# Kernel tuning notes

Hardware: AMD Instinct MI355X
Metric: run time of the kernel (lower is better)

The kernel has to match this reference:

```python
import jax, jax.numpy as jnp
import numpy as np
from jax import lax
from jax.scipy.special import logsumexp

NUM_CLASSES = 170
ALPHA = 0.2
B, T = 16, 8192


def setup_inputs() -> dict:
    key = jax.random.key(0)
    logits = jax.random.normal(key, (B, T, NUM_CLASSES), dtype=jnp.float32)
    # transition matrix: alpha on diagonal, uniform off-diagonal
    off = (1.0 - ALPHA) / (NUM_CLASSES - 1)
    trans = jnp.full((NUM_CLASSES, NUM_CLASSES), off, dtype=jnp.float32)
    trans = trans.at[jnp.arange(NUM_CLASSES), jnp.arange(NUM_CLASSES)].set(ALPHA)
    init = jnp.full((NUM_CLASSES,), 1.0 / NUM_CLASSES, dtype=jnp.float32)
    return {"logits": logits, "transition_matrix": trans, "initial_distribution": init}


def reference(logits, transition_matrix, initial_distribution):
    eps = 1e-12
    log_T = jnp.log(transition_matrix + eps)          # (C, C)
    log_init = jnp.log(initial_distribution + eps)    # (C,)
    log_probs = jax.nn.log_softmax(logits, axis=-1)   # (B, T, C)
    Bn, Tn, C = log_probs.shape
    lp = jnp.moveaxis(log_probs, 1, 0)                # (T, B, C) time-major for scan

    # forward recursion: alpha_t[j] = logsumexp_i(alpha_{t-1}[i] + logT[i,j]) + lp_t[j]
    alpha0 = log_init[None, :] + lp[0]                # (B, C)

    def fwd_step(a_prev, lp_t):
        a = logsumexp(a_prev[:, :, None] + log_T[None, :, :], axis=1) + lp_t
        return a, a

    _, alpha_rest = lax.scan(fwd_step, alpha0, lp[1:])
    alpha = jnp.concatenate([alpha0[None], alpha_rest], axis=0)  # (T, B, C)

    # backward recursion: beta_t[i] = logsumexp_j(logT[i,j] + lp_{t+1}[j] + beta_{t+1}[j])
    betaT = jnp.zeros((Bn, C), dtype=log_probs.dtype)

    def bwd_step(b_next, lp_next):
        b = logsumexp(log_T[None, :, :] + (lp_next + b_next)[:, None, :], axis=2)
        return b, b

    _, beta_rest = lax.scan(bwd_step, betaT, lp[1:], reverse=True)
    beta = jnp.concatenate([beta_rest, betaT[None]], axis=0)     # (T, B, C)

    posterior = jax.nn.softmax(alpha + beta, axis=-1)            # (T, B, C)
    return jnp.moveaxis(posterior, 0, 1)                         # (B, T, C)
```

## Files before the change

kernel.cpp:

```cpp
#include <hip/hip_runtime.h>
#include <hip/hip_fp16.h>


#define NCLS 170
#define BB 16
#define TT 8192
#define LCH 32
#define WARM 16
#define NCHUNK (TT / LCH)

struct Row { float x, y, z; };

__device__ __forceinline__ float wave_sum_b(float x) {
  x += __int_as_float(__builtin_amdgcn_update_dpp(0, __float_as_int(x), 0x111, 0xF, 0xF, true));
  x += __int_as_float(__builtin_amdgcn_update_dpp(0, __float_as_int(x), 0x112, 0xF, 0xF, true));
  x += __int_as_float(__builtin_amdgcn_update_dpp(0, __float_as_int(x), 0x114, 0xF, 0xF, true));
  x += __int_as_float(__builtin_amdgcn_update_dpp(0, __float_as_int(x), 0x118, 0xF, 0xF, true));
  x += __int_as_float(__builtin_amdgcn_update_dpp(0, __float_as_int(x), 0x142, 0xA, 0xF, true));
  x += __int_as_float(__builtin_amdgcn_update_dpp(0, __float_as_int(x), 0x143, 0xC, 0xF, true));
  return __int_as_float(__builtin_amdgcn_readlane(__float_as_int(x), 63));
}

__global__ __launch_bounds__(64, 4) void hmm_fb(const float* __restrict__ logits,
                                                const float* __restrict__ trans,
                                                const float* __restrict__ initd,
                                                float* __restrict__ out) {
  __shared__ __half2 pb01[LCH * 64];
  const int lane = threadIdx.x;

  const int d = blockIdx.x;
  const int o = (d & 7) * (BB * NCHUNK / 8) + (d >> 3);
  const int b = o / NCHUNK;
  const int chunk = o % NCHUNK;
  const int t0 = chunk * LCH;
  const int t1 = t0 + LCH;

  const float off = trans[1] + 1e-12f;
  const float dia = trans[0] + 1e-12f;
  const float dd = dia - off;

  const int c0 = lane, c1 = lane + 64, c2 = lane + 128;
  const bool cok = (c2 < NCLS);
  const float* lg = logits + (size_t)b * TT * NCLS;

  auto ldraw = [&](int t) -> Row {
    const float* r = lg + (size_t)t * NCLS;
    Row w;
    w.x = r[c0];
    w.y = r[c1];
    w.z = cok ? r[c2] : 0.f;
    return w;
  };
  auto eRow = [&](const Row& w) -> Row {
    Row e;
    e.x = __expf(w.x);
    e.y = __expf(w.y);
    e.z = cok ? __expf(w.z) : 0.f;
    return e;
  };

  __half2 ph2[LCH / 2];

  float v0, v1, v2s;
  auto fcore = [&](const Row& e, float& u0, float& u1, float& u2) -> float {
    u0 = v0 * e.x; u1 = v1 * e.y; u2 = v2s * e.z;
    float S = wave_sum_b(u0 + u1 + u2);
    float os = off * S;
    v0 = __fmaf_rn(dd, u0, os);
    v1 = __fmaf_rn(dd, u1, os);
    v2s = __fmaf_rn(dd, u2, os);
    return S;
  };

  Row r0, r1, r2, r3;
  if (t0 == 0) {
    v0 = initd[c0]; v1 = initd[c1]; v2s = cok ? initd[c2] : 0.f;
    r0 = ldraw(0); r1 = ldraw(1); r2 = ldraw(2); r3 = ldraw(3);
  } else {
    v0 = 1.f; v1 = 1.f; v2s = cok ? 1.f : 0.f;
    const int ts = t0 - WARM;
    r0 = ldraw(ts); r1 = ldraw(ts + 1); r2 = ldraw(ts + 2); r3 = ldraw(ts + 3);
#pragma unroll
    for (int g = 0; g < WARM / 4; ++g) {
      const int tn = ts + 4 * g + 4;
      Row n0 = ldraw(tn), n1 = ldraw(tn + 1), n2 = ldraw(tn + 2), n3 = ldraw(tn + 3);
      Row e0 = eRow(r0), e1 = eRow(r1), e2 = eRow(r2), e3 = eRow(r3);
      float u0, u1, u2;
      fcore(e0, u0, u1, u2);
      fcore(e1, u0, u1, u2);
      fcore(e2, u0, u1, u2);
      float S3 = fcore(e3, u0, u1, u2);
      float rs = __builtin_amdgcn_rcpf(S3);
      v0 *= rs; v1 *= rs; v2s *= rs;
      r0 = n0; r1 = n1; r2 = n2; r3 = n3;
    }
  }

#define FGROUP(i)                                                              \
  {                                                                            \
    const int tn = t0 + (i) + 4;                                               \
    Row n0 = ldraw(tn + 0 > TT - 1 ? TT - 1 : tn + 0);                         \
    Row n1 = ldraw(tn + 1 > TT - 1 ? TT - 1 : tn + 1);                         \
    Row n2 = ldraw(tn + 2 > TT - 1 ? TT - 1 : tn + 2);                         \
    Row n3 = ldraw(tn + 3 > TT - 1 ? TT - 1 : tn + 3);                         \
    Row e0 = eRow(r0), e1 = eRow(r1), e2 = eRow(r2), e3 = eRow(r3);            \
    float u0, u1, u2;                                                          \
    float S0 = fcore(e0, u0, u1, u2);                                          \
    float x0 = __builtin_amdgcn_rcpf(S0);                                      \
    pb01[((i) + 0) * 64 + lane] = __floats2half2_rn(u0 * x0, u1 * x0);         \
    __half pa = __float2half(u2 * x0);                                         \
    float S1 = fcore(e1, u0, u1, u2);                                          \
    float x1 = __builtin_amdgcn_rcpf(S1);                                      \
    pb01[((i) + 1) * 64 + lane] = __floats2half2_rn(u0 * x1, u1 * x1);         \
    ph2[(i) / 2] = __halves2half2(pa, __float2half(u2 * x1));                  \
    float S2 = fcore(e2, u0, u1, u2);                                          \
    float x2 = __builtin_amdgcn_rcpf(S2);                                      \
    pb01[((i) + 2) * 64 + lane] = __floats2half2_rn(u0 * x2, u1 * x2);         \
    __half pb = __float2half(u2 * x2);                                         \
    float S3 = fcore(e3, u0, u1, u2);                                          \
    float x3 = __builtin_amdgcn_rcpf(S3);                                      \
    pb01[((i) + 3) * 64 + lane] = __floats2half2_rn(u0 * x3, u1 * x3);         \
    ph2[(i) / 2 + 1] = __halves2half2(pb, __float2half(u2 * x3));              \
    v0 *= x3; v1 *= x3; v2s *= x3;          \
    r0 = n0; r1 = n1; r2 = n2; r3 = n3;                                        \
  }

  FGROUP(0) FGROUP(4) FGROUP(8) FGROUP(12)
  FGROUP(16) FGROUP(20) FGROUP(24) FGROUP(28)
#undef FGROUP

  float q0 = 1.f, q1 = 1.f, q2 = cok ? 1.f : 0.f;
  int te2 = t1 + WARM;
  if (te2 > TT) te2 = TT;

  auto ldB = [&](int tp1) -> Row {
    int rr = tp1 < 0 ? 0 : (tp1 > TT - 1 ? TT - 1 : tp1);
    Row w = ldraw(rr);
    if (tp1 >= TT) { w.x = 0.f; w.y = 0.f; w.z = 0.f; }
    return w;
  };
  auto bcore = [&](const Row& e) -> float {
    float w0 = e.x * q0, w1 = e.y * q1, w2 = e.z * q2;
    float S = wave_sum_b(w0 + w1 + w2);
    float os = off * S;
    q0 = __fmaf_rn(dd, w0, os);
    q1 = __fmaf_rn(dd, w1, os);
    q2 = __fmaf_rn(dd, w2, os);
    return S;
  };

  r0 = ldB(te2); r1 = ldB(te2 - 1); r2 = ldB(te2 - 2); r3 = ldB(te2 - 3);

  for (int t = te2 - 1; t > t1 - 1; t -= 4) {
    Row n0 = ldB(t - 3), n1 = ldB(t - 4), n2 = ldB(t - 5), n3 = ldB(t - 6);
    Row e0 = eRow(r0), e1 = eRow(r1), e2 = eRow(r2), e3 = eRow(r3);
    bcore(e0); bcore(e1); bcore(e2);
    float S3 = bcore(e3);
    float rs = __builtin_amdgcn_rcpf(S3);
    q0 *= rs; q1 *= rs; q2 *= rs;
    r0 = n0; r1 = n1; r2 = n2; r3 = n3;
  }

#define WPOST(tt, ta)                                                          \
  {                                                                            \
    __half2 h01 = pb01[(tt) * 64 + lane];                                      \
    float a0 = __low2float(h01) * q0;                                          \
    float a1 = __high2float(h01) * q1;                                         \
    __half2 h2v = ph2[(tt) >> 1];                                              \
    float p2f = ((tt) & 1) ? __high2float(h2v) : __low2float(h2v);             \
    float a2 = cok ? p2f * q2 : 0.f;                                           \
    float z = wave_sum_b(a0 + a1 + a2);                                        \
    float iz = __builtin_amdgcn_rcpf(z);                                       \
    float* op = out + ((size_t)b * TT + (ta)) * NCLS;                          \
    op[c0] = a0 * iz;                                                          \
    op[c1] = a1 * iz;                                                          \
    if (cok) op[c2] = a2 * iz;                                                 \
  }

#define BGROUP(i)                                                              \
  {                                                                            \
    const int t = t1 - 1 - (i);                                                \
    Row n0 = ldB(t - 3), n1 = ldB(t - 4), n2 = ldB(t - 5), n3 = ldB(t - 6);    \
    Row e0 = eRow(r0), e1 = eRow(r1), e2 = eRow(r2), e3 = eRow(r3);            \
    bcore(e0); WPOST(LCH - 1 - (i), t)                                         \
    bcore(e1); WPOST(LCH - 2 - (i), t - 1)                                     \
    bcore(e2); WPOST(LCH - 3 - (i), t - 2)                                     \
    float S3 = bcore(e3); WPOST(LCH - 4 - (i), t - 3)                          \
    float rs = __builtin_amdgcn_rcpf(S3);                                      \
    q0 *= rs; q1 *= rs; q2 *= rs;                                              \
    r0 = n0; r1 = n1; r2 = n2; r3 = n3;                                        \
  }

  BGROUP(0) BGROUP(4) BGROUP(8) BGROUP(12)
  BGROUP(16) BGROUP(20) BGROUP(24) BGROUP(28)
#undef BGROUP
#undef WPOST
}

extern "C" void kernel_launch(void* const* d_in, const int* in_sizes, int n_in,
                              void* d_out, int out_size, void* d_ws, size_t ws_size,
                              hipStream_t stream) {
  const float* logits = (const float*)d_in[0];
  const float* trans  = (const float*)d_in[1];
  const float* initd  = (const float*)d_in[2];
  float* out = (float*)d_out;
  dim3 grid(BB * NCHUNK);
  dim3 block(64);
  hipLaunchKernelGGL(hmm_fb, grid, block, 0, stream, logits, trans, initd, out);
}
```

Baseline: 59.65 us.

## Vectorize row loads/stores as float2 and deepen prefetch to two groups

Changes the class-to-lane mapping so each lane loads and stores classes 2*lane and 2*lane+1 as a single float2, with a scalar tail for classes 128..169. Also doubles the register prefetch depth from one 4-row group to two (a/b rotation) in both the forward and backward passes. Warm-up loops become runtime-bounded, and the load clamps now stay inside the chunk. The goal is fewer memory instructions and more latency hiding on the serial recurrence, at the cost of more registers under launch_bounds(64,4).

```diff
diff --git a/kernel.cpp b/kernel.cpp
--- a/kernel.cpp
+++ b/kernel.cpp
@@ -39,16 +39,16 @@
   const float dia = trans[0] + 1e-12f;
   const float dd = dia - off;
 
-  const int c0 = lane, c1 = lane + 64, c2 = lane + 128;
-  const bool cok = (c2 < NCLS);
+  const bool cok = (lane < NCLS - 128);
   const float* lg = logits + (size_t)b * TT * NCLS;
 
   auto ldraw = [&](int t) -> Row {
     const float* r = lg + (size_t)t * NCLS;
+    float2 xy = *(const float2*)(r + 2 * lane);
     Row w;
-    w.x = r[c0];
-    w.y = r[c1];
-    w.z = cok ? r[c2] : 0.f;
+    w.x = xy.x;
+    w.y = xy.y;
+    w.z = cok ? r[128 + lane] : 0.f;
     return w;
   };
   auto eRow = [&](const Row& w) -> Row {
@@ -72,38 +72,42 @@
     return S;
   };
 
-  Row r0, r1, r2, r3;
+  Row a0, a1, a2, a3, b0, b1, b2, b3;
+  int ts;
   if (t0 == 0) {
-    v0 = initd[c0]; v1 = initd[c1]; v2s = cok ? initd[c2] : 0.f;
-    r0 = ldraw(0); r1 = ldraw(1); r2 = ldraw(2); r3 = ldraw(3);
+    ts = 0;
+    float2 i01 = *(const float2*)(initd + 2 * lane);
+    v0 = i01.x; v1 = i01.y; v2s = cok ? initd[128 + lane] : 0.f;
   } else {
+    ts = t0 - WARM;
     v0 = 1.f; v1 = 1.f; v2s = cok ? 1.f : 0.f;
-    const int ts = t0 - WARM;
-    r0 = ldraw(ts); r1 = ldraw(ts + 1); r2 = ldraw(ts + 2); r3 = ldraw(ts + 3);
-#pragma unroll
-    for (int g = 0; g < WARM / 4; ++g) {
-      const int tn = ts + 4 * g + 4;
-      Row n0 = ldraw(tn), n1 = ldraw(tn + 1), n2 = ldraw(tn + 2), n3 = ldraw(tn + 3);
-      Row e0 = eRow(r0), e1 = eRow(r1), e2 = eRow(r2), e3 = eRow(r3);
-      float u0, u1, u2;
-      fcore(e0, u0, u1, u2);
-      fcore(e1, u0, u1, u2);
-      fcore(e2, u0, u1, u2);
-      float S3 = fcore(e3, u0, u1, u2);
-      float rs = __builtin_amdgcn_rcpf(S3);
-      v0 *= rs; v1 *= rs; v2s *= rs;
-      r0 = n0; r1 = n1; r2 = n2; r3 = n3;
-    }
+  }
+  a0 = ldraw(ts); a1 = ldraw(ts + 1); a2 = ldraw(ts + 2); a3 = ldraw(ts + 3);
+  b0 = ldraw(ts + 4); b1 = ldraw(ts + 5); b2 = ldraw(ts + 6); b3 = ldraw(ts + 7);
+
+  for (int g = 0; g < (t0 - ts) / 4; ++g) {
+    const int tn = ts + 8 + 4 * g;
+    Row n0 = ldraw(tn), n1 = ldraw(tn + 1), n2 = ldraw(tn + 2), n3 = ldraw(tn + 3);
+    Row e0 = eRow(a0), e1 = eRow(a1), e2 = eRow(a2), e3 = eRow(a3);
+    float u0, u1, u2;
+    fcore(e0, u0, u1, u2);
+    fcore(e1, u0, u1, u2);
+    fcore(e2, u0, u1, u2);
+    float S3 = fcore(e3, u0, u1, u2);
+    float rs = __builtin_amdgcn_rcpf(S3);
+    v0 *= rs; v1 *= rs; v2s *= rs;
+    a0 = b0; a1 = b1; a2 = b2; a3 = b3;
+    b0 = n0; b1 = n1; b2 = n2; b3 = n3;
   }
 
 #define FGROUP(i)                                                              \
   {                                                                            \
-    const int tn = t0 + (i) + 4;                                               \
-    Row n0 = ldraw(tn + 0 > TT - 1 ? TT - 1 : tn + 0);                         \
-    Row n1 = ldraw(tn + 1 > TT - 1 ? TT - 1 : tn + 1);                         \
-    Row n2 = ldraw(tn + 2 > TT - 1 ? TT - 1 : tn + 2);                         \
-    Row n3 = ldraw(tn + 3 > TT - 1 ? TT - 1 : tn + 3);                         \
-    Row e0 = eRow(r0), e1 = eRow(r1), e2 = eRow(r2), e3 = eRow(r3);            \
+    const int tn = t0 + (i) + 8;                                               \
+    Row n0 = ldraw(tn + 0 > t1 - 1 ? t1 - 1 : tn + 0);                         \
+    Row n1 = ldraw(tn + 1 > t1 - 1 ? t1 - 1 : tn + 1);                         \
+    Row n2 = ldraw(tn + 2 > t1 - 1 ? t1 - 1 : tn + 2);                         \
+    Row n3 = ldraw(tn + 3 > t1 - 1 ? t1 - 1 : tn + 3);                         \
+    Row e0 = eRow(a0), e1 = eRow(a1), e2 = eRow(a2), e3 = eRow(a3);            \
     float u0, u1, u2;                                                          \
     float S0 = fcore(e0, u0, u1, u2);                                          \
     float x0 = __builtin_amdgcn_rcpf(S0);                                      \
@@ -122,7 +126,8 @@
     pb01[((i) + 3) * 64 + lane] = __floats2half2_rn(u0 * x3, u1 * x3);         \
     ph2[(i) / 2 + 1] = __halves2half2(pb, __float2half(u2 * x3));              \
     v0 *= x3; v1 *= x3; v2s *= x3;          \
-    r0 = n0; r1 = n1; r2 = n2; r3 = n3;                                        \
+    a0 = b0; a1 = b1; a2 = b2; a3 = b3;                                        \
+    b0 = n0; b1 = n1; b2 = n2; b3 = n3;                                        \
   }
 
   FGROUP(0) FGROUP(4) FGROUP(8) FGROUP(12)
@@ -132,6 +137,7 @@
   float q0 = 1.f, q1 = 1.f, q2 = cok ? 1.f : 0.f;
   int te2 = t1 + WARM;
   if (te2 > TT) te2 = TT;
+  const int tstart = te2 - 1;
 
   auto ldB = [&](int tp1) -> Row {
     int rr = tp1 < 0 ? 0 : (tp1 > TT - 1 ? TT - 1 : tp1);
@@ -149,46 +155,54 @@
     return S;
   };
 
-  r0 = ldB(te2); r1 = ldB(te2 - 1); r2 = ldB(te2 - 2); r3 = ldB(te2 - 3);
-
-  for (int t = te2 - 1; t > t1 - 1; t -= 4) {
-    Row n0 = ldB(t - 3), n1 = ldB(t - 4), n2 = ldB(t - 5), n3 = ldB(t - 6);
-    Row e0 = eRow(r0), e1 = eRow(r1), e2 = eRow(r2), e3 = eRow(r3);
+  a0 = ldB(tstart + 1); a1 = ldB(tstart); a2 = ldB(tstart - 1); a3 = ldB(tstart - 2);
+  b0 = ldB(tstart - 3); b1 = ldB(tstart - 4); b2 = ldB(tstart - 5); b3 = ldB(tstart - 6);
+
+  for (int g = 0; g < (te2 - t1) / 4; ++g) {
+    const int tp = tstart - 7 - 4 * g;
+    Row n0 = ldB(tp), n1 = ldB(tp - 1), n2 = ldB(tp - 2), n3 = ldB(tp - 3);
+    Row e0 = eRow(a0), e1 = eRow(a1), e2 = eRow(a2), e3 = eRow(a3);
     bcore(e0); bcore(e1); bcore(e2);
     float S3 = bcore(e3);
     float rs = __builtin_amdgcn_rcpf(S3);
     q0 *= rs; q1 *= rs; q2 *= rs;
-    r0 = n0; r1 = n1; r2 = n2; r3 = n3;
+    a0 = b0; a1 = b1; a2 = b2; a3 = b3;
+    b0 = n0; b1 = n1; b2 = n2; b3 = n3;
   }
 
 #define WPOST(tt, ta)                                                          \
   {                                                                            \
     __half2 h01 = pb01[(tt) * 64 + lane];                                      \
-    float a0 = __low2float(h01) * q0;                                          \
-    float a1 = __high2float(h01) * q1;                                         \
+    float g0 = __low2float(h01) * q0;                                          \
+    float g1 = __high2float(h01) * q1;                                         \
     __half2 h2v = ph2[(tt) >> 1];                                              \
     float p2f = ((tt) & 1) ? __high2float(h2v) : __low2float(h2v);             \
-    float a2 = cok ? p2f * q2 : 0.f;                                           \
-    float z = wave_sum_b(a0 + a1 + a2);                                        \
+    float g2 = cok ? p2f * q2 : 0.f;                                           \
+    float z = wave_sum_b(g0 + g1 + g2);                                        \
     float iz = __builtin_amdgcn_rcpf(z);                                       \
     float* op = out + ((size_t)b * TT + (ta)) * NCLS;                          \
-    op[c0] = a0 * iz;                                                          \
-    op[c1] = a1 * iz;                                                          \
-    if (cok) op[c2] = a2 * iz;                                                 \
+    float2 o01; o01.x = g0 * iz; o01.y = g1 * iz;                              \
+    *(float2*)(op + 2 * lane) = o01;                                           \
+    if (cok) op[128 + lane] = g2 * iz;                                         \
   }
 
 #define BGROUP(i)                                                              \
   {                                                                            \
+    const int tp = t1 - 8 - (i);                  \
+    Row n0 = ldB(tp + 0 < t0 + 1 ? t0 + 1 : tp + 0);                           \
+    Row n1 = ldB(tp - 1 < t0 + 1 ? t0 + 1 : tp - 1);                           \
+    Row n2 = ldB(tp - 2 < t0 + 1 ? t0 + 1 : tp - 2);                           \
+    Row n3 = ldB(tp - 3 < t0 + 1 ? t0 + 1 : tp - 3);                           \
+    Row e0 = eRow(a0), e1 = eRow(a1), e2 = eRow(a2), e3 = eRow(a3);            \
     const int t = t1 - 1 - (i);                                                \
-    Row n0 = ldB(t - 3), n1 = ldB(t - 4), n2 = ldB(t - 5), n3 = ldB(t - 6);    \
-    Row e0 = eRow(r0), e1 = eRow(r1), e2 = eRow(r2), e3 = eRow(r3);            \
     bcore(e0); WPOST(LCH - 1 - (i), t)                                         \
     bcore(e1); WPOST(LCH - 2 - (i), t - 1)                                     \
     bcore(e2); WPOST(LCH - 3 - (i), t - 2)                                     \
     float S3 = bcore(e3); WPOST(LCH - 4 - (i), t - 3)                          \
     float rs = __builtin_amdgcn_rcpf(S3);                                      \
     q0 *= rs; q1 *= rs; q2 *= rs;                                              \
-    r0 = n0; r1 = n1; r2 = n2; r3 = n3;                                        \
+    a0 = b0; a1 = b1; a2 = b2; a3 = b3;                                        \
+    b0 = n0; b1 = n1; b2 = n2; b3 = n3;                                        \
   }
 
   BGROUP(0) BGROUP(4) BGROUP(8) BGROUP(12)
```

Measured after the change: 59.02 us. About the same (-1.0%).
